# Kernel tuning notes

Measured on AMD Instinct MI355X. Metric: run time of the kernel, lower is better.

Reference implementation:

```python
import jax, jax.numpy as jnp
import numpy as np

L, B, S, D, H, DQ, DH = 6, 2, 1024, 1024, 16, 64, 4096  # layers, batch, seq, d_e, heads, d_q, d_h
EPS = 1e-5


def _ln(x, g, b):
    m = jnp.mean(x, axis=-1, keepdims=True)
    v = jnp.mean(jnp.square(x - m), axis=-1, keepdims=True)
    return (x - m) / jnp.sqrt(v + EPS) * g + b


def setup_inputs() -> dict:
    key = jax.random.key(0)
    ks = jax.random.split(key, 8)
    f = lambda k, shape: (jax.random.normal(k, shape, jnp.float32) * 0.02)
    return {
        "x": jax.random.normal(ks[0], (B, S, D), jnp.float32),
        "mask": jnp.zeros((B, S, S), dtype=bool),
        "Wq": f(ks[1], (L, D, H * DQ)), "bq": jnp.zeros((L, H * DQ), jnp.float32),
        "Wk": f(ks[2], (L, D, H * DQ)), "bk": jnp.zeros((L, H * DQ), jnp.float32),
        "Wv": f(ks[3], (L, D, H * DQ)), "bv": jnp.zeros((L, H * DQ), jnp.float32),
        "Wo": f(ks[4], (L, H * DQ, D)), "bo": jnp.zeros((L, D), jnp.float32),
        "ln1_g": jnp.ones((L, D), jnp.float32), "ln1_b": jnp.zeros((L, D), jnp.float32),
        "W1": f(ks[5], (L, D, DH)), "b1": jnp.zeros((L, DH), jnp.float32),
        "W2": f(ks[6], (L, DH, D)), "b2": jnp.zeros((L, D), jnp.float32),
        "ln2_g": jnp.ones((L, D), jnp.float32), "ln2_b": jnp.zeros((L, D), jnp.float32),
    }


def _encoder(x, mask, Wq, bq, Wk, bk, Wv, bv, Wo, bo, ln1_g, ln1_b, W1, b1, W2, b2, ln2_g, ln2_b):
    scale = 1.0 / np.sqrt(DQ).astype(np.float32)

    def step(h, p):
        wq, q_b, wk, k_b, wv, v_b, wo, o_b, g1, be1, w1, f_b1, w2, f_b2, g2, be2 = p
        q = (h @ wq + q_b).reshape(B, S, H, DQ)
        k = (h @ wk + k_b).reshape(B, S, H, DQ)
        v = (h @ wv + v_b).reshape(B, S, H, DQ)
        scores = jnp.einsum('bqhd,bkhd->bhqk', q, k) * scale  # [B,H,S,S]
        scores = jnp.where(mask[:, None, :, :], jnp.float32(-1e9), scores)
        attn = jax.nn.softmax(scores, axis=-1)
        ctx = jnp.einsum('bhqk,bkhd->bqhd', attn, v).reshape(B, S, H * DQ)
        h = _ln(h + ctx @ wo + o_b, g1, be1)
        ff = jax.nn.relu(h @ w1 + f_b1) @ w2 + f_b2  # 1x1 conv1d FFN == pointwise MLP
        h = _ln(h + ff, g2, be2)
        return h, None

    params = (Wq, bq, Wk, bk, Wv, bv, Wo, bo, ln1_g, ln1_b, W1, b1, W2, b2, ln2_g, ln2_b)
    out, _ = jax.lax.scan(step, x, params)
    return out


def reference(x, mask, Wq, bq, Wk, bk, Wv, bv, Wo, bo, ln1_g, ln1_b, W1, b1, W2, b2, ln2_g, ln2_b):
    return _encoder(x, mask, Wq, bq, Wk, bk, Wv, bv, Wo, bo, ln1_g, ln1_b, W1, b1, W2, b2, ln2_g, ln2_b)
```

## Files before the change

### kernel.cpp

```cpp
#include <hip/hip_runtime.h>


typedef unsigned short u16;
typedef __attribute__((ext_vector_type(8))) short bh8;
typedef __attribute__((ext_vector_type(4))) float f32x4;

#define PLANE (2048ull * 1024ull)

__device__ __forceinline__ u16 f2b(float f) {
    unsigned u = __float_as_uint(f);
    u += 0x7fffu + ((u >> 16) & 1u);
    return (u16)(u >> 16);
}
__device__ __forceinline__ void gl_lds16(const void* g, void* l) {
    __builtin_amdgcn_global_load_lds((const __attribute__((address_space(1))) void*)g,
                                     (__attribute__((address_space(3))) void*)l, 16, 0, 0);
}

#define MFMA(a, b, c) __builtin_amdgcn_mfma_f32_16x16x32_bf16((a), (b), (c), 0, 0, 0)

__global__ __launch_bounds__(256) void init_h(const float* __restrict__ x,
                                              u16* __restrict__ hbf, float* __restrict__ hf, int n) {
    int i = blockIdx.x * 256 + threadIdx.x;
    if (i < n) { float v = x[i]; hbf[i] = f2b(v); hf[i] = v; }
}

__device__ __forceinline__ void tp_tile_f2b(const float* __restrict__ in, u16* __restrict__ out,
                                            int R, int C, int ty, int tx) {
    const int r0 = ty * 64, c0 = tx * 64;
    __shared__ alignas(16) u16 tile[64][72];
    const int tid = threadIdx.x;
#pragma unroll
    for (int it = 0; it < 4; ++it) {
        int s = it * 256 + tid;
        int rr = s >> 4, c4 = (s & 15) * 4;
        const float* p = &in[(size_t)(r0 + rr) * C + c0 + c4];
        float d0 = p[0], d1 = p[1], d2 = p[2], d3 = p[3];
        u16 t[4] = { f2b(d0), f2b(d1), f2b(d2), f2b(d3) };
        *(ushort4*)&tile[rr][c4] = *(const ushort4*)t;
    }
    __syncthreads();
#pragma unroll
    for (int it = 0; it < 2; ++it) {
        int chunk = it * 256 + tid, cc = chunk >> 3, r8 = chunk & 7;
        u16 tmp[8];
#pragma unroll
        for (int j = 0; j < 8; ++j) tmp[j] = tile[r8 * 8 + j][cc];
        *(uint4*)&out[(size_t)(c0 + cc) * R + r0 + r8 * 8] = *(const uint4*)tmp;
    }
}

__global__ __launch_bounds__(256) void transpose_weights(
        const float* __restrict__ Wq, const float* __restrict__ Wk,
        const float* __restrict__ Wv, const float* __restrict__ Wo,
        const float* __restrict__ W1, const float* __restrict__ W2,
        u16* __restrict__ WqT, u16* __restrict__ WkT, u16* __restrict__ WvT,
        u16* __restrict__ WoT, u16* __restrict__ W1T, u16* __restrict__ W2T) {
    int t = blockIdx.x;
    if (t < 1024) {
        int wsel = t >> 8, u = t & 255;
        const float* src = wsel == 0 ? Wq : wsel == 1 ? Wk : wsel == 2 ? Wv : Wo;
        u16* dst = wsel == 0 ? WqT : wsel == 1 ? WkT : wsel == 2 ? WvT : WoT;
        tp_tile_f2b(src, dst, 1024, 1024, u >> 4, u & 15);
    } else if (t < 2048) {
        int u = t - 1024;
        tp_tile_f2b(W1, W1T, 1024, 4096, u >> 6, u & 63);
    } else {
        int u = t - 2048;
        tp_tile_f2b(W2, W2T, 4096, 1024, u >> 4, u & 15);
    }
}

__device__ __forceinline__ void gemm_loop64(const u16* __restrict__ A, const u16* __restrict__ BT,
                                            int K, int kb, int ke, int bm, int bn, f32x4 acc[2][4]) {
    __shared__ alignas(16) u16 As[128 * 64];
    __shared__ alignas(16) u16 Bs[64 * 64];
    const int tid = threadIdx.x;
    const int lane = tid & 63, wave = tid >> 6;
    const int quad = lane >> 4, l16 = lane & 15;

    for (int k0 = kb; k0 < ke; k0 += 64) {
        __syncthreads();
#pragma unroll
        for (int it = 0; it < 4; ++it) {
            int chunk = it * 256 + tid;
            int row = chunk >> 3, sseg = (chunk & 7) ^ (row & 7);
            gl_lds16(A + (size_t)(bm + row) * K + k0 + sseg * 8, As + chunk * 8);
        }
#pragma unroll
        for (int it = 0; it < 2; ++it) {
            int chunk = it * 256 + tid;
            int row = chunk >> 3, sseg = (chunk & 7) ^ (row & 7);
            gl_lds16(BT + (size_t)(bn + row) * K + k0 + sseg * 8, Bs + chunk * 8);
        }
        __syncthreads();

#pragma unroll
        for (int ks = 0; ks < 2; ++ks) {
            bh8 af[2], bf[4];
#pragma unroll
            for (int mi = 0; mi < 2; ++mi) {
                int row = wave * 32 + mi * 16 + l16;
                af[mi] = *(const bh8*)&As[row * 64 + ((ks * 4 + quad) ^ (l16 & 7)) * 8];
            }
#pragma unroll
            for (int ni = 0; ni < 4; ++ni) {
                int row = ni * 16 + l16;
                bf[ni] = *(const bh8*)&Bs[row * 64 + ((ks * 4 + quad) ^ (l16 & 7)) * 8];
            }
#pragma unroll
            for (int mi = 0; mi < 2; ++mi)
#pragma unroll
                for (int ni = 0; ni < 4; ++ni)
                    acc[mi][ni] = MFMA(af[mi], bf[ni], acc[mi][ni]);
        }
    }
}

__global__ __launch_bounds__(256) void qkv_gemm(const u16* __restrict__ A,
        const u16* __restrict__ BTq, const u16* __restrict__ BTk, const u16* __restrict__ BTv,
        const float* __restrict__ bq, const float* __restrict__ bk, const float* __restrict__ bv,
        u16* __restrict__ Oq, u16* __restrict__ Ok, u16* __restrict__ OvT) {
    const int z = blockIdx.z;
    const u16* BT = z == 0 ? BTq : (z == 1 ? BTk : BTv);
    const float* bias = z == 0 ? bq : (z == 1 ? bk : bv);
    const int bm = blockIdx.y * 128, bn = blockIdx.x * 64;
    f32x4 acc[2][4] = {};
    gemm_loop64(A, BT, 1024, 0, 1024, bm, bn, acc);

    const int lane = threadIdx.x & 63, wave = threadIdx.x >> 6;
    const int quad = lane >> 4, l16 = lane & 15;
    const float scale = (z == 0) ? 0.125f : 1.0f;
#pragma unroll
    for (int mi = 0; mi < 2; ++mi) {
        int row0 = bm + wave * 32 + mi * 16 + quad * 4;
#pragma unroll
        for (int ni = 0; ni < 4; ++ni) {
            int col = bn + ni * 16 + l16;
            float bv_ = bias[col];
            if (z < 2) {
                u16* O = z == 0 ? Oq : Ok;
#pragma unroll
                for (int r = 0; r < 4; ++r)
                    O[(size_t)(row0 + r) * 1024 + col] = f2b((acc[mi][ni][r] + bv_) * scale);
            } else {
                int b = row0 >> 10, s0 = row0 & 1023;
                u16 tmp[4];
#pragma unroll
                for (int r = 0; r < 4; ++r) tmp[r] = f2b(acc[mi][ni][r] + bv_);
                *(ushort4*)&OvT[(size_t)(b * 1024 + col) * 1024 + s0] = *(const ushort4*)tmp;
            }
        }
    }
}

__global__ __launch_bounds__(256) void gemm_relu(const u16* __restrict__ A, const u16* __restrict__ BT,
        const float* __restrict__ bias, u16* __restrict__ Cb, int N, int K) {
    const int bm = blockIdx.y * 128, bn = blockIdx.x * 64;
    f32x4 acc[2][4] = {};
    gemm_loop64(A, BT, K, 0, K, bm, bn, acc);
    const int lane = threadIdx.x & 63, wave = threadIdx.x >> 6;
    const int quad = lane >> 4, l16 = lane & 15;
#pragma unroll
    for (int mi = 0; mi < 2; ++mi) {
        int row0 = bm + wave * 32 + mi * 16 + quad * 4;
#pragma unroll
        for (int ni = 0; ni < 4; ++ni) {
            int col = bn + ni * 16 + l16;
            float bv = bias[col];
#pragma unroll
            for (int r = 0; r < 4; ++r)
                Cb[(size_t)(row0 + r) * N + col] = f2b(fmaxf(acc[mi][ni][r] + bv, 0.0f));
        }
    }
}

__global__ __launch_bounds__(256) void gemm_splitk(const u16* __restrict__ A, const u16* __restrict__ BT,
        float* __restrict__ P, int K, int slice) {
    const int bm = blockIdx.y * 128, bn = blockIdx.x * 64, s = blockIdx.z;
    f32x4 acc[2][4] = {};
    gemm_loop64(A, BT, K, s * slice, (s + 1) * slice, bm, bn, acc);
    float* Pl = P + (size_t)s * PLANE;
    const int lane = threadIdx.x & 63, wave = threadIdx.x >> 6;
    const int quad = lane >> 4, l16 = lane & 15;
#pragma unroll
    for (int mi = 0; mi < 2; ++mi) {
        int row0 = bm + wave * 32 + mi * 16 + quad * 4;
#pragma unroll
        for (int ni = 0; ni < 4; ++ni) {
            int col = bn + ni * 16 + l16;
#pragma unroll
            for (int r = 0; r < 4; ++r)
                Pl[(size_t)(row0 + r) * 1024 + col] = acc[mi][ni][r];
        }
    }
}

__global__ __launch_bounds__(256) void attn_kernel(const u16* __restrict__ q, const u16* __restrict__ k,
        const u16* __restrict__ vT, const unsigned char* __restrict__ mask, u16* __restrict__ ctx) {
    __shared__ alignas(16) u16 Qs[64 * 64];
    __shared__ alignas(16) u16 Ks[64 * 64];
    __shared__ alignas(16) u16 VTs[64 * 64];
    __shared__ alignas(16) u16 Ps[4][16 * 64];
    const int tid = threadIdx.x, lane = tid & 63, wave = tid >> 6;
    const int quad = lane >> 4, l16 = lane & 15;
    const int bh = blockIdx.y, b = bh >> 4, h = bh & 15;
    const int q0 = blockIdx.x * 64;

#pragma unroll
    for (int i = 0; i < 2; ++i) {
        int chunk = i * 256 + tid, rr = chunk >> 3, seg = (chunk & 7) ^ (rr & 7);
        gl_lds16(q + (size_t)(b * 1024 + q0 + rr) * 1024 + h * 64 + seg * 8, Qs + chunk * 8);
    }

    float l[4] = {0.0f, 0.0f, 0.0f, 0.0f};
    f32x4 o[4] = {};

    for (int kv0 = 0; kv0 < 1024; kv0 += 64) {
        __syncthreads();
#pragma unroll
        for (int i = 0; i < 2; ++i) {
            int chunk = i * 256 + tid, rr = chunk >> 3, seg = (chunk & 7) ^ (rr & 7);
            gl_lds16(k + (size_t)(b * 1024 + kv0 + rr) * 1024 + h * 64 + seg * 8, Ks + chunk * 8);
            gl_lds16(vT + (size_t)(bh * 64 + rr) * 1024 + kv0 + seg * 8, VTs + chunk * 8);
        }
        __syncthreads();

        f32x4 st[4] = {};
#pragma unroll
        for (int ks = 0; ks < 2; ++ks) {
            bh8 a = *(const bh8*)&Qs[(wave * 16 + l16) * 64 + ((ks * 4 + quad) ^ (l16 & 7)) * 8];
#pragma unroll
            for (int ni = 0; ni < 4; ++ni) {
                bh8 bb = *(const bh8*)&Ks[(ni * 16 + l16) * 64 + ((ks * 4 + quad) ^ (l16 & 7)) * 8];
                st[ni] = MFMA(a, bb, st[ni]);
            }
        }

#pragma unroll
        for (int r = 0; r < 4; ++r) {
            int qg = q0 + wave * 16 + quad * 4 + r;
            int prow = quad * 4 + r;
            float p[4], rs = 0.0f;
#pragma unroll
            for (int ni = 0; ni < 4; ++ni) {
                float sv = st[ni][r];
                int kg = kv0 + ni * 16 + l16;
                if (mask[(size_t)b * 1048576 + (size_t)qg * 1024 + kg]) sv = -1e9f;
                p[ni] = __expf(sv);
                rs += p[ni];
            }
#pragma unroll
            for (int off = 1; off < 16; off <<= 1) rs += __shfl_xor(rs, off, 64);
            l[r] += rs;
#pragma unroll
            for (int ni = 0; ni < 4; ++ni) {
                int cchunk = ((ni * 2) + (l16 >> 3)) ^ (prow & 7);
                Ps[wave][prow * 64 + cchunk * 8 + (l16 & 7)] = f2b(p[ni]);
            }
        }
        __syncthreads();

#pragma unroll
        for (int ks = 0; ks < 2; ++ks) {
            bh8 a = *(const bh8*)&Ps[wave][l16 * 64 + ((ks * 4 + quad) ^ (l16 & 7)) * 8];
#pragma unroll
            for (int ni = 0; ni < 4; ++ni) {
                bh8 bb = *(const bh8*)&VTs[(ni * 16 + l16) * 64 + ((ks * 4 + quad) ^ (l16 & 7)) * 8];
                o[ni] = MFMA(a, bb, o[ni]);
            }
        }
    }

#pragma unroll
    for (int r = 0; r < 4; ++r) {
        float inv = 1.0f / l[r];
#pragma unroll
        for (int ni = 0; ni < 4; ++ni) {
            size_t idx = (size_t)(b * 1024 + q0 + wave * 16 + quad * 4 + r) * 1024 + h * 64 + ni * 16 + l16;
            ctx[idx] = f2b(o[ni][r] * inv);
        }
    }
}

__global__ __launch_bounds__(256) void ln_reduce(const float* __restrict__ P, int np,
        const float* __restrict__ bias, const float* __restrict__ res,
        const float* __restrict__ g, const float* __restrict__ bb,
        u16* __restrict__ outb, float* __restrict__ outf) {
    const int row = blockIdx.x, tid = threadIdx.x;
    const int lane = tid & 63, wave = tid >> 6;
    float v[4], s = 0.0f, sq = 0.0f;
#pragma unroll
    for (int i = 0; i < 4; ++i) {
        int col = tid + i * 256;
        size_t idx = (size_t)row * 1024 + col;
        float t = bias[col] + res[idx];
        for (int p = 0; p < np; ++p) t += P[(size_t)p * PLANE + idx];
        v[i] = t; s += t; sq += t * t;
    }
#pragma unroll
    for (int off = 32; off > 0; off >>= 1) { s += __shfl_down(s, off, 64); sq += __shfl_down(sq, off, 64); }
    __shared__ float ps[4], pq[4];
    if (lane == 0) { ps[wave] = s; pq[wave] = sq; }
    __syncthreads();
    s = ps[0] + ps[1] + ps[2] + ps[3];
    sq = pq[0] + pq[1] + pq[2] + pq[3];
    const float mean = s * (1.0f / 1024.0f);
    const float var = sq * (1.0f / 1024.0f) - mean * mean;
    const float rstd = rsqrtf(var + 1e-5f);
#pragma unroll
    for (int i = 0; i < 4; ++i) {
        int col = tid + i * 256;
        float y = (v[i] - mean) * rstd * g[col] + bb[col];
        size_t idx = (size_t)row * 1024 + col;
        outb[idx] = f2b(y);
        outf[idx] = y;
    }
}

extern "C" void kernel_launch(void* const* d_in, const int* in_sizes, int n_in,
                              void* d_out, int out_size, void* d_ws, size_t ws_size,
                              hipStream_t stream) {
    const float* x  = (const float*)d_in[0];
    const unsigned char* mask = (const unsigned char*)d_in[1];
    const float* Wq = (const float*)d_in[2];
    const float* bq = (const float*)d_in[3];
    const float* Wk = (const float*)d_in[4];
    const float* bk = (const float*)d_in[5];
    const float* Wv = (const float*)d_in[6];
    const float* bv = (const float*)d_in[7];
    const float* Wo = (const float*)d_in[8];
    const float* bo = (const float*)d_in[9];
    const float* g1 = (const float*)d_in[10];
    const float* be1= (const float*)d_in[11];
    const float* W1 = (const float*)d_in[12];
    const float* b1 = (const float*)d_in[13];
    const float* W2 = (const float*)d_in[14];
    const float* b2 = (const float*)d_in[15];
    const float* g2 = (const float*)d_in[16];
    const float* be2= (const float*)d_in[17];

    char* w = (char*)d_ws;
    const size_t MB = 1ull << 20;
    if (ws_size < 104 * MB) return;

    float* hf  = (float*)(w + 0 * MB);
    u16*   hbf = (u16*)  (w + 8 * MB);
    u16*   Qb  = (u16*)  (w + 12 * MB);
    u16*   Kb  = (u16*)  (w + 16 * MB);
    u16*   VTb = (u16*)  (w + 24 * MB);
    u16*   CTX = (u16*)  (w + 28 * MB);
    u16*   FF  = (u16*)  (w + 32 * MB);
    u16*   WqT = (u16*)  (w + 48 * MB);
    u16*   WkT = (u16*)  (w + 50 * MB);
    u16*   WvT = (u16*)  (w + 52 * MB);
    u16*   WoT = (u16*)  (w + 54 * MB);
    u16*   W1T = (u16*)  (w + 56 * MB);
    u16*   W2T = (u16*)  (w + 64 * MB);
    float* Pp  = (float*)(w + 72 * MB);

    init_h<<<8192, 256, 0, stream>>>(x, hbf, hf, 2048 * 1024);

    for (int l = 0; l < 6; ++l) {
        const size_t wOff = (size_t)l * 1024 * 1024;
        const size_t fOff = (size_t)l * 1024 * 4096;

        transpose_weights<<<3072, 256, 0, stream>>>(Wq + wOff, Wk + wOff, Wv + wOff, Wo + wOff,
                W1 + fOff, W2 + fOff, WqT, WkT, WvT, WoT, W1T, W2T);
        qkv_gemm<<<dim3(16, 16, 3), 256, 0, stream>>>(hbf, WqT, WkT, WvT,
                bq + l * 1024, bk + l * 1024, bv + l * 1024, Qb, Kb, VTb);
        attn_kernel<<<dim3(16, 32), 256, 0, stream>>>(Qb, Kb, VTb, mask, CTX);
        gemm_splitk<<<dim3(16, 16, 2), 256, 0, stream>>>(CTX, WoT, Pp, 1024, 512);
        ln_reduce<<<2048, 256, 0, stream>>>(Pp, 2, bo + l * 1024, hf,
                g1 + l * 1024, be1 + l * 1024, hbf, hf);
        gemm_relu<<<dim3(64, 16), 256, 0, stream>>>(hbf, W1T, b1 + l * 4096, FF, 4096, 1024);
        gemm_splitk<<<dim3(16, 16, 4), 256, 0, stream>>>(FF, W2T, Pp, 4096, 1024);
        float* outf = (l == 5) ? (float*)d_out : hf;
        ln_reduce<<<2048, 256, 0, stream>>>(Pp, 4, b2 + l * 1024, hf,
                g2 + l * 1024, be2 + l * 1024, hbf, outf);
    }
}
```

Baseline: 1.203 ms.

## Double-buffer GEMM and attention tiles, batch weight transposes, remap blocks to XCDs, vectorize LN

GEMM main loop and attention KV loop now use double-buffered LDS, so the next tile's global-to-LDS load is issued while the current tile is being computed. All six layers' weight transposes run in one launch into a larger workspace instead of one launch per layer. Block IDs are remapped so neighbouring tiles land on the same XCD for L2 reuse. LayerNorm and init are vectorized to float4. LDS use doubles, which may lower occupancy, and the required workspace grows to 248MB.

```diff
diff --git a/kernel.cpp b/kernel.cpp
--- a/kernel.cpp
+++ b/kernel.cpp
@@ -19,10 +19,23 @@
 
 #define MFMA(a, b, c) __builtin_amdgcn_mfma_f32_16x16x32_bf16((a), (b), (c), 0, 0, 0)
 
+__device__ __forceinline__ void xcd_remap(int nx, int& bx, int& by) {
+    int id = blockIdx.y * nx + blockIdx.x;
+    int cpx = (nx * gridDim.y) >> 3;
+    int sid = (id & 7) * cpx + (id >> 3);
+    bx = sid & (nx - 1);
+    by = sid / nx;
+}
+
 __global__ __launch_bounds__(256) void init_h(const float* __restrict__ x,
-                                              u16* __restrict__ hbf, float* __restrict__ hf, int n) {
+                                              u16* __restrict__ hbf, float* __restrict__ hf, int n4) {
     int i = blockIdx.x * 256 + threadIdx.x;
-    if (i < n) { float v = x[i]; hbf[i] = f2b(v); hf[i] = v; }
+    if (i < n4) {
+        float4 v = ((const float4*)x)[i];
+        ((float4*)hf)[i] = v;
+        u16 t[4] = { f2b(v.x), f2b(v.y), f2b(v.z), f2b(v.w) };
+        ((ushort4*)hbf)[i] = *(const ushort4*)t;
+    }
 }
 
 __device__ __forceinline__ void tp_tile_f2b(const float* __restrict__ in, u16* __restrict__ out,
@@ -54,66 +67,91 @@
         const float* __restrict__ Wq, const float* __restrict__ Wk,
         const float* __restrict__ Wv, const float* __restrict__ Wo,
         const float* __restrict__ W1, const float* __restrict__ W2,
-        u16* __restrict__ WqT, u16* __restrict__ WkT, u16* __restrict__ WvT,
-        u16* __restrict__ WoT, u16* __restrict__ W1T, u16* __restrict__ W2T) {
-    int t = blockIdx.x;
-    if (t < 1024) {
-        int wsel = t >> 8, u = t & 255;
-        const float* src = wsel == 0 ? Wq : wsel == 1 ? Wk : wsel == 2 ? Wv : Wo;
-        u16* dst = wsel == 0 ? WqT : wsel == 1 ? WkT : wsel == 2 ? WvT : WoT;
-        tp_tile_f2b(src, dst, 1024, 1024, u >> 4, u & 15);
-    } else if (t < 2048) {
-        int u = t - 1024;
-        tp_tile_f2b(W1, W1T, 1024, 4096, u >> 6, u & 63);
+        u16* __restrict__ WT) {
+    const int t = blockIdx.x;
+    const int l = t / 3072, u = t - l * 3072;
+    const size_t M1 = 1024ull * 1024ull;
+    const float* wq = Wq + (size_t)l * M1;
+    const float* wk = Wk + (size_t)l * M1;
+    const float* wv = Wv + (size_t)l * M1;
+    const float* wo = Wo + (size_t)l * M1;
+    const float* w1 = W1 + (size_t)l * 4 * M1;
+    const float* w2 = W2 + (size_t)l * 4 * M1;
+    u16* base = WT + (size_t)l * 12 * M1;
+    if (u < 1024) {
+        int wsel = u >> 8, uu = u & 255;
+        const float* src = wsel == 0 ? wq : wsel == 1 ? wk : wsel == 2 ? wv : wo;
+        u16* dst = base + (size_t)wsel * M1;
+        tp_tile_f2b(src, dst, 1024, 1024, uu >> 4, uu & 15);
+    } else if (u < 2048) {
+        int uu = u - 1024;
+        tp_tile_f2b(w1, base + 4 * M1, 1024, 4096, uu >> 6, uu & 63);
     } else {
-        int u = t - 2048;
-        tp_tile_f2b(W2, W2T, 4096, 1024, u >> 4, u & 15);
+        int uu = u - 2048;
+        tp_tile_f2b(w2, base + 8 * M1, 4096, 1024, uu >> 4, uu & 15);
+    }
+}
+
+__device__ __forceinline__ void stage_ab(const u16* const ap[4], const u16* const bp[2],
+                                         int koff, u16* As, u16* Bs, int tid) {
+#pragma unroll
+    for (int it = 0; it < 4; ++it) gl_lds16(ap[it] + koff, As + (it * 256 + tid) * 8);
+#pragma unroll
+    for (int it = 0; it < 2; ++it) gl_lds16(bp[it] + koff, Bs + (it * 256 + tid) * 8);
+}
+
+__device__ __forceinline__ void gemm_compute(const u16* As, const u16* Bs,
+                                             int wave, int quad, int l16, f32x4 acc[2][4]) {
+#pragma unroll
+    for (int ks = 0; ks < 2; ++ks) {
+        bh8 af[2], bf[4];
+#pragma unroll
+        for (int mi = 0; mi < 2; ++mi)
+            af[mi] = *(const bh8*)&As[(wave * 32 + mi * 16 + l16) * 64 + ((ks * 4 + quad) ^ (l16 & 7)) * 8];
+#pragma unroll
+        for (int ni = 0; ni < 4; ++ni)
+            bf[ni] = *(const bh8*)&Bs[(ni * 16 + l16) * 64 + ((ks * 4 + quad) ^ (l16 & 7)) * 8];
+#pragma unroll
+        for (int mi = 0; mi < 2; ++mi)
+#pragma unroll
+            for (int ni = 0; ni < 4; ++ni)
+                acc[mi][ni] = MFMA(af[mi], bf[ni], acc[mi][ni]);
     }
 }
 
 __device__ __forceinline__ void gemm_loop64(const u16* __restrict__ A, const u16* __restrict__ BT,
                                             int K, int kb, int ke, int bm, int bn, f32x4 acc[2][4]) {
-    __shared__ alignas(16) u16 As[128 * 64];
-    __shared__ alignas(16) u16 Bs[64 * 64];
+    __shared__ alignas(16) u16 As0[128 * 64];
+    __shared__ alignas(16) u16 Bs0[64 * 64];
+    __shared__ alignas(16) u16 As1[128 * 64];
+    __shared__ alignas(16) u16 Bs1[64 * 64];
     const int tid = threadIdx.x;
     const int lane = tid & 63, wave = tid >> 6;
     const int quad = lane >> 4, l16 = lane & 15;
 
-    for (int k0 = kb; k0 < ke; k0 += 64) {
+    const u16* ap[4];
+    const u16* bp[2];
+#pragma unroll
+    for (int it = 0; it < 4; ++it) {
+        int chunk = it * 256 + tid, row = chunk >> 3, sseg = (chunk & 7) ^ (row & 7);
+        ap[it] = A + (size_t)(bm + row) * K + kb + sseg * 8;
+    }
+#pragma unroll
+    for (int it = 0; it < 2; ++it) {
+        int chunk = it * 256 + tid, row = chunk >> 3, sseg = (chunk & 7) ^ (row & 7);
+        bp[it] = BT + (size_t)(bn + row) * K + kb + sseg * 8;
+    }
+
+    stage_ab(ap, bp, 0, As0, Bs0, tid);
+    __syncthreads();
+    for (int k0 = kb; k0 < ke; k0 += 128) {
+        stage_ab(ap, bp, k0 + 64 - kb, As1, Bs1, tid);
+        gemm_compute(As0, Bs0, wave, quad, l16, acc);
         __syncthreads();
-#pragma unroll
-        for (int it = 0; it < 4; ++it) {
-            int chunk = it * 256 + tid;
-            int row = chunk >> 3, sseg = (chunk & 7) ^ (row & 7);
-            gl_lds16(A + (size_t)(bm + row) * K + k0 + sseg * 8, As + chunk * 8);
-        }
-#pragma unroll
-        for (int it = 0; it < 2; ++it) {
-            int chunk = it * 256 + tid;
-            int row = chunk >> 3, sseg = (chunk & 7) ^ (row & 7);
-            gl_lds16(BT + (size_t)(bn + row) * K + k0 + sseg * 8, Bs + chunk * 8);
-        }
-        __syncthreads();
-
-#pragma unroll
-        for (int ks = 0; ks < 2; ++ks) {
-            bh8 af[2], bf[4];
-#pragma unroll
-            for (int mi = 0; mi < 2; ++mi) {
-                int row = wave * 32 + mi * 16 + l16;
-                af[mi] = *(const bh8*)&As[row * 64 + ((ks * 4 + quad) ^ (l16 & 7)) * 8];
-            }
-#pragma unroll
-            for (int ni = 0; ni < 4; ++ni) {
-                int row = ni * 16 + l16;
-                bf[ni] = *(const bh8*)&Bs[row * 64 + ((ks * 4 + quad) ^ (l16 & 7)) * 8];
-            }
-#pragma unroll
-            for (int mi = 0; mi < 2; ++mi)
-#pragma unroll
-                for (int ni = 0; ni < 4; ++ni)
-                    acc[mi][ni] = MFMA(af[mi], bf[ni], acc[mi][ni]);
-        }
+        const bool more = (k0 + 128) < ke;
+        if (more) stage_ab(ap, bp, k0 + 128 - kb, As0, Bs0, tid);
+        gemm_compute(As1, Bs1, wave, quad, l16, acc);
+        if (more) __syncthreads();
     }
 }
 
@@ -121,10 +159,12 @@
         const u16* __restrict__ BTq, const u16* __restrict__ BTk, const u16* __restrict__ BTv,
         const float* __restrict__ bq, const float* __restrict__ bk, const float* __restrict__ bv,
         u16* __restrict__ Oq, u16* __restrict__ Ok, u16* __restrict__ OvT) {
+    int bx, by;
+    xcd_remap(16, bx, by);
     const int z = blockIdx.z;
     const u16* BT = z == 0 ? BTq : (z == 1 ? BTk : BTv);
     const float* bias = z == 0 ? bq : (z == 1 ? bk : bv);
-    const int bm = blockIdx.y * 128, bn = blockIdx.x * 64;
+    const int bm = by * 128, bn = bx * 64;
     f32x4 acc[2][4] = {};
     gemm_loop64(A, BT, 1024, 0, 1024, bm, bn, acc);
 
@@ -156,7 +196,9 @@
 
 __global__ __launch_bounds__(256) void gemm_relu(const u16* __restrict__ A, const u16* __restrict__ BT,
         const float* __restrict__ bias, u16* __restrict__ Cb, int N, int K) {
-    const int bm = blockIdx.y * 128, bn = blockIdx.x * 64;
+    int bx, by;
+    xcd_remap(64, bx, by);
+    const int bm = by * 128, bn = bx * 64;
     f32x4 acc[2][4] = {};
     gemm_loop64(A, BT, K, 0, K, bm, bn, acc);
     const int lane = threadIdx.x & 63, wave = threadIdx.x >> 6;
@@ -177,7 +219,9 @@
 
 __global__ __launch_bounds__(256) void gemm_splitk(const u16* __restrict__ A, const u16* __restrict__ BT,
         float* __restrict__ P, int K, int slice) {
-    const int bm = blockIdx.y * 128, bn = blockIdx.x * 64, s = blockIdx.z;
+    int bx, by;
+    xcd_remap(16, bx, by);
+    const int bm = by * 128, bn = bx * 64, s = blockIdx.z;
     f32x4 acc[2][4] = {};
     gemm_loop64(A, BT, K, s * slice, (s + 1) * slice, bm, bn, acc);
     float* Pl = P + (size_t)s * PLANE;
@@ -196,80 +240,107 @@
     }
 }
 
+__device__ __forceinline__ void attn_stageK(const u16* k, int b, int h, int kv0, u16* Ks) {
+    const int tid = threadIdx.x;
+#pragma unroll
+    for (int i = 0; i < 2; ++i) {
+        int chunk = i * 256 + tid, rr = chunk >> 3, seg = (chunk & 7) ^ (rr & 7);
+        gl_lds16(k + (size_t)(b * 1024 + kv0 + rr) * 1024 + h * 64 + seg * 8, Ks + chunk * 8);
+    }
+}
+__device__ __forceinline__ void attn_stageV(const u16* vT, int bh, int kv0, u16* VTs) {
+    const int tid = threadIdx.x;
+#pragma unroll
+    for (int i = 0; i < 2; ++i) {
+        int chunk = i * 256 + tid, rr = chunk >> 3, seg = (chunk & 7) ^ (rr & 7);
+        gl_lds16(vT + (size_t)(bh * 64 + rr) * 1024 + kv0 + seg * 8, VTs + chunk * 8);
+    }
+}
+
+__device__ __forceinline__ void attn_tile(const u16* Qs, const u16* Ksc, const u16* VTsc,
+        u16* Ksn, u16* VTsn, u16* Psw, const u16* k, const u16* vT,
+        const unsigned char* __restrict__ mask, int b, int h, int bh, int q0, int kv0, bool pre,
+        int wave, int quad, int l16, float l[4], f32x4 o[4]) {
+    if (pre) attn_stageK(k, b, h, kv0 + 64, Ksn);
+
+    f32x4 st[4] = {};
+#pragma unroll
+    for (int ks = 0; ks < 2; ++ks) {
+        bh8 a = *(const bh8*)&Qs[(wave * 16 + l16) * 64 + ((ks * 4 + quad) ^ (l16 & 7)) * 8];
+#pragma unroll
+        for (int ni = 0; ni < 4; ++ni) {
+            bh8 bb = *(const bh8*)&Ksc[(ni * 16 + l16) * 64 + ((ks * 4 + quad) ^ (l16 & 7)) * 8];
+            st[ni] = MFMA(a, bb, st[ni]);
+        }
+    }
+
+#pragma unroll
+    for (int r = 0; r < 4; ++r) {
+        int qg = q0 + wave * 16 + quad * 4 + r;
+        int prow = quad * 4 + r;
+        float p[4], rs = 0.0f;
+#pragma unroll
+        for (int ni = 0; ni < 4; ++ni) {
+            float sv = st[ni][r];
+            int kg = kv0 + ni * 16 + l16;
+            if (mask[(size_t)b * 1048576 + (size_t)qg * 1024 + kg]) sv = -1e9f;
+            p[ni] = __expf(sv);
+            rs += p[ni];
+        }
+#pragma unroll
+        for (int off = 1; off < 16; off <<= 1) rs += __shfl_xor(rs, off, 64);
+        l[r] += rs;
+#pragma unroll
+        for (int ni = 0; ni < 4; ++ni) {
+            int cchunk = ((ni * 2) + (l16 >> 3)) ^ (prow & 7);
+            Psw[prow * 64 + cchunk * 8 + (l16 & 7)] = f2b(p[ni]);
+        }
+    }
+    __syncthreads();
+    if (pre) attn_stageV(vT, bh, kv0 + 64, VTsn);
+
+#pragma unroll
+    for (int ks = 0; ks < 2; ++ks) {
+        bh8 a = *(const bh8*)&Psw[l16 * 64 + ((ks * 4 + quad) ^ (l16 & 7)) * 8];
+#pragma unroll
+        for (int ni = 0; ni < 4; ++ni) {
+            bh8 bb = *(const bh8*)&VTsc[(ni * 16 + l16) * 64 + ((ks * 4 + quad) ^ (l16 & 7)) * 8];
+            o[ni] = MFMA(a, bb, o[ni]);
+        }
+    }
+}
+
 __global__ __launch_bounds__(256) void attn_kernel(const u16* __restrict__ q, const u16* __restrict__ k,
         const u16* __restrict__ vT, const unsigned char* __restrict__ mask, u16* __restrict__ ctx) {
     __shared__ alignas(16) u16 Qs[64 * 64];
-    __shared__ alignas(16) u16 Ks[64 * 64];
-    __shared__ alignas(16) u16 VTs[64 * 64];
+    __shared__ alignas(16) u16 Ks0[64 * 64];
+    __shared__ alignas(16) u16 Ks1[64 * 64];
+    __shared__ alignas(16) u16 VTs0[64 * 64];
+    __shared__ alignas(16) u16 VTs1[64 * 64];
     __shared__ alignas(16) u16 Ps[4][16 * 64];
     const int tid = threadIdx.x, lane = tid & 63, wave = tid >> 6;
     const int quad = lane >> 4, l16 = lane & 15;
-    const int bh = blockIdx.y, b = bh >> 4, h = bh & 15;
-    const int q0 = blockIdx.x * 64;
+    int bx, by;
+    xcd_remap(16, bx, by);
+    const int bh = by, b = bh >> 4, h = bh & 15;
+    const int q0 = bx * 64;
 
 #pragma unroll
     for (int i = 0; i < 2; ++i) {
         int chunk = i * 256 + tid, rr = chunk >> 3, seg = (chunk & 7) ^ (rr & 7);
         gl_lds16(q + (size_t)(b * 1024 + q0 + rr) * 1024 + h * 64 + seg * 8, Qs + chunk * 8);
     }
+    attn_stageK(k, b, h, 0, Ks0);
+    attn_stageV(vT, bh, 0, VTs0);
+    __syncthreads();
 
     float l[4] = {0.0f, 0.0f, 0.0f, 0.0f};
     f32x4 o[4] = {};
-
-    for (int kv0 = 0; kv0 < 1024; kv0 += 64) {
-        __syncthreads();
-#pragma unroll
-        for (int i = 0; i < 2; ++i) {
-            int chunk = i * 256 + tid, rr = chunk >> 3, seg = (chunk & 7) ^ (rr & 7);
-            gl_lds16(k + (size_t)(b * 1024 + kv0 + rr) * 1024 + h * 64 + seg * 8, Ks + chunk * 8);
-            gl_lds16(vT + (size_t)(bh * 64 + rr) * 1024 + kv0 + seg * 8, VTs + chunk * 8);
-        }
-        __syncthreads();
-
-        f32x4 st[4] = {};
-#pragma unroll
-        for (int ks = 0; ks < 2; ++ks) {
-            bh8 a = *(const bh8*)&Qs[(wave * 16 + l16) * 64 + ((ks * 4 + quad) ^ (l16 & 7)) * 8];
-#pragma unroll
-            for (int ni = 0; ni < 4; ++ni) {
-                bh8 bb = *(const bh8*)&Ks[(ni * 16 + l16) * 64 + ((ks * 4 + quad) ^ (l16 & 7)) * 8];
-                st[ni] = MFMA(a, bb, st[ni]);
-            }
-        }
-
-#pragma unroll
-        for (int r = 0; r < 4; ++r) {
-            int qg = q0 + wave * 16 + quad * 4 + r;
-            int prow = quad * 4 + r;
-            float p[4], rs = 0.0f;
-#pragma unroll
-            for (int ni = 0; ni < 4; ++ni) {
-                float sv = st[ni][r];
-                int kg = kv0 + ni * 16 + l16;
-                if (mask[(size_t)b * 1048576 + (size_t)qg * 1024 + kg]) sv = -1e9f;
-                p[ni] = __expf(sv);
-                rs += p[ni];
-            }
-#pragma unroll
-            for (int off = 1; off < 16; off <<= 1) rs += __shfl_xor(rs, off, 64);
-            l[r] += rs;
-#pragma unroll
-            for (int ni = 0; ni < 4; ++ni) {
-                int cchunk = ((ni * 2) + (l16 >> 3)) ^ (prow & 7);
-                Ps[wave][prow * 64 + cchunk * 8 + (l16 & 7)] = f2b(p[ni]);
-            }
-        }
-        __syncthreads();
-
-#pragma unroll
-        for (int ks = 0; ks < 2; ++ks) {
-            bh8 a = *(const bh8*)&Ps[wave][l16 * 64 + ((ks * 4 + quad) ^ (l16 & 7)) * 8];
-#pragma unroll
-            for (int ni = 0; ni < 4; ++ni) {
-                bh8 bb = *(const bh8*)&VTs[(ni * 16 + l16) * 64 + ((ks * 4 + quad) ^ (l16 & 7)) * 8];
-                o[ni] = MFMA(a, bb, o[ni]);
-            }
-        }
+    for (int kv0 = 0; kv0 < 1024; kv0 += 128) {
+        attn_tile(Qs, Ks0, VTs0, Ks1, VTs1, Ps[wave], k, vT, mask, b, h, bh, q0,
+                  kv0, true, wave, quad, l16, l, o);
+        attn_tile(Qs, Ks1, VTs1, Ks0, VTs0, Ps[wave], k, vT, mask, b, h, bh, q0,
+                  kv0 + 64, (kv0 + 128) < 1024, wave, quad, l16, l, o);
     }
 
 #pragma unroll
@@ -289,15 +360,17 @@
         u16* __restrict__ outb, float* __restrict__ outf) {
     const int row = blockIdx.x, tid = threadIdx.x;
     const int lane = tid & 63, wave = tid >> 6;
-    float v[4], s = 0.0f, sq = 0.0f;
-#pragma unroll
-    for (int i = 0; i < 4; ++i) {
-        int col = tid + i * 256;
-        size_t idx = (size_t)row * 1024 + col;
-        float t = bias[col] + res[idx];
-        for (int p = 0; p < np; ++p) t += P[(size_t)p * PLANE + idx];
-        v[i] = t; s += t; sq += t * t;
-    }
+    const int c4 = tid * 4;
+    const size_t base = (size_t)row * 1024 + c4;
+    float4 t = *(const float4*)&res[base];
+    float4 bi = *(const float4*)&bias[c4];
+    t.x += bi.x; t.y += bi.y; t.z += bi.z; t.w += bi.w;
+    for (int p = 0; p < np; ++p) {
+        float4 q = *(const float4*)&P[(size_t)p * PLANE + base];
+        t.x += q.x; t.y += q.y; t.z += q.z; t.w += q.w;
+    }
+    float s = t.x + t.y + t.z + t.w;
+    float sq = t.x * t.x + t.y * t.y + t.z * t.z + t.w * t.w;
 #pragma unroll
     for (int off = 32; off > 0; off >>= 1) { s += __shfl_down(s, off, 64); sq += __shfl_down(sq, off, 64); }
     __shared__ float ps[4], pq[4];
@@ -308,14 +381,15 @@
     const float mean = s * (1.0f / 1024.0f);
     const float var = sq * (1.0f / 1024.0f) - mean * mean;
     const float rstd = rsqrtf(var + 1e-5f);
-#pragma unroll
-    for (int i = 0; i < 4; ++i) {
-        int col = tid + i * 256;
-        float y = (v[i] - mean) * rstd * g[col] + bb[col];
-        size_t idx = (size_t)row * 1024 + col;
-        outb[idx] = f2b(y);
-        outf[idx] = y;
-    }
+    float4 gg = *(const float4*)&g[c4];
+    float4 bv = *(const float4*)&bb[c4];
+    float y0 = (t.x - mean) * rstd * gg.x + bv.x;
+    float y1 = (t.y - mean) * rstd * gg.y + bv.y;
+    float y2 = (t.z - mean) * rstd * gg.z + bv.z;
+    float y3 = (t.w - mean) * rstd * gg.w + bv.w;
+    *(float4*)&outf[base] = make_float4(y0, y1, y2, y3);
+    u16 ob[4] = { f2b(y0), f2b(y1), f2b(y2), f2b(y3) };
+    *(ushort4*)&outb[base] = *(const ushort4*)ob;
 }
 
 extern "C" void kernel_launch(void* const* d_in, const int* in_sizes, int n_in,
@@ -342,7 +416,7 @@
 
     char* w = (char*)d_ws;
     const size_t MB = 1ull << 20;
-    if (ws_size < 104 * MB) return;
+    if (ws_size < 248 * MB) return;
 
     float* hf  = (float*)(w + 0 * MB);
     u16*   hbf = (u16*)  (w + 8 * MB);
@@ -351,22 +425,22 @@
     u16*   VTb = (u16*)  (w + 24 * MB);
     u16*   CTX = (u16*)  (w + 28 * MB);
     u16*   FF  = (u16*)  (w + 32 * MB);
-    u16*   WqT = (u16*)  (w + 48 * MB);
-    u16*   WkT = (u16*)  (w + 50 * MB);
-    u16*   WvT = (u16*)  (w + 52 * MB);
-    u16*   WoT = (u16*)  (w + 54 * MB);
-    u16*   W1T = (u16*)  (w + 56 * MB);
-    u16*   W2T = (u16*)  (w + 64 * MB);
     float* Pp  = (float*)(w + 72 * MB);
-
-    init_h<<<8192, 256, 0, stream>>>(x, hbf, hf, 2048 * 1024);
-
+    u16*   WT6 = (u16*)  (w + 104 * MB);
+
+    init_h<<<2048, 256, 0, stream>>>(x, hbf, hf, 512 * 1024);
+    transpose_weights<<<18432, 256, 0, stream>>>(Wq, Wk, Wv, Wo, W1, W2, WT6);
+
+    const size_t M1 = 1024ull * 1024ull;
     for (int l = 0; l < 6; ++l) {
-        const size_t wOff = (size_t)l * 1024 * 1024;
-        const size_t fOff = (size_t)l * 1024 * 4096;
-
-        transpose_weights<<<3072, 256, 0, stream>>>(Wq + wOff, Wk + wOff, Wv + wOff, Wo + wOff,
-                W1 + fOff, W2 + fOff, WqT, WkT, WvT, WoT, W1T, W2T);
+        u16* base = WT6 + (size_t)l * 12 * M1;
+        u16* WqT = base;
+        u16* WkT = base + 1 * M1;
+        u16* WvT = base + 2 * M1;
+        u16* WoT = base + 3 * M1;
+        u16* W1T = base + 4 * M1;
+        u16* W2T = base + 8 * M1;
+
         qkv_gemm<<<dim3(16, 16, 3), 256, 0, stream>>>(hbf, WqT, WkT, WvT,
                 bq + l * 1024, bk + l * 1024, bv + l * 1024, Qb, Kb, VTb);
         attn_kernel<<<dim3(16, 32), 256, 0, stream>>>(Qb, Kb, VTb, mask, CTX);
```

Result: slower. 1.266 ms (+5.3%).
